# Kernel tuning notes

Measured on AMD Instinct MI355X. Metric: run time of the kernel, lower is better.

Reference implementation:

```python
import jax, jax.numpy as jnp
import numpy as np

N = 200000   # nodes
E = 6400000  # edges (avg degree 32)
F_IN = 128
N_CLASSES = 4
DIMS = [F_IN, 24, 12, 6, 4, 2]


def setup_inputs() -> dict:
    key = jax.random.key(0)
    ks = jax.random.split(key, 16)
    inp = {}
    inp['x'] = jax.random.normal(ks[0], (N, F_IN), dtype=jnp.float32)
    inp['edge_index'] = jax.random.randint(ks[1], (2, E), 0, N, dtype=jnp.int32)
    for i in range(5):
        fan_in = DIMS[i]
        inp[f'W{i+1}'] = jax.random.normal(ks[2 + i], (DIMS[i], DIMS[i + 1]), dtype=jnp.float32) / np.float32(np.sqrt(fan_in))
        inp[f'b{i+1}'] = jnp.zeros((DIMS[i + 1],), dtype=jnp.float32)
    inp['Wc'] = jax.random.normal(ks[8], (2, N_CLASSES), dtype=jnp.float32) / np.float32(np.sqrt(2.0))
    inp['bc'] = jnp.zeros((N_CLASSES,), dtype=jnp.float32)
    return inp


def _gcn_forward(x, row, col, norm, weights, biases, Wc, bc):
    h = x
    for W, b in zip(weights, biases):
        xl = h @ W                               # [N, d_out] linear transform first (d_out <= d_in)
        msg = norm[:, None] * xl[row]            # gather + normalize: [E+N, d_out]
        agg = jax.ops.segment_max(msg, col, num_segments=N)  # aggr='max'
        h = jnp.tanh(agg + b)
    out = h @ Wc + bc
    return out, h


def reference(x, edge_index, W1, b1, W2, b2, W3, b3, W4, b4, W5, b5, Wc, bc):
    loops = jnp.arange(N, dtype=edge_index.dtype)
    row = jnp.concatenate([edge_index[0], loops])  # source (with self loops)
    col = jnp.concatenate([edge_index[1], loops])  # target
    # symmetric GCN normalization on A + I
    deg = jax.ops.segment_sum(jnp.ones_like(col, dtype=jnp.float32), col, num_segments=N)
    dinv = jnp.where(deg > 0, jax.lax.rsqrt(deg), 0.0)
    norm = dinv[row] * dinv[col]                   # [E+N]
    weights = [W1, W2, W3, W4, W5]
    biases = [b1, b2, b3, b4, b5]
    return _gcn_forward(x, row, col, norm, weights, biases, Wc, bc)
```

## Files before the change

### kernel.cpp

```cpp
#include <hip/hip_runtime.h>
#include <cmath>

#define NN 200000
#define EE 6400000
#define CSH 8
#define BSZ 256
#define NBKT 782
#define GRID_A 512
#define BLK_A 256
#define RB_SHIFT 13
#define NRB 25

__device__ __forceinline__ unsigned int fenc(float f) {
    unsigned int u = __float_as_uint(f);
    return (u & 0x80000000u) ? ~u : (u | 0x80000000u);
}
__device__ __forceinline__ float fdec(unsigned int u) {
    unsigned int v = (u & 0x80000000u) ? (u & 0x7FFFFFFFu) : ~u;
    return __uint_as_float(v);
}


__global__ __launch_bounds__(BLK_A) void count_buckets_kernel(const int* __restrict__ col,
                                                              int* __restrict__ blkhist) {
    __shared__ int h[NBKT];
    for (int t = threadIdx.x; t < NBKT; t += BLK_A) h[t] = 0;
    __syncthreads();
    const int4* col4 = (const int4*)col;
    for (int i = blockIdx.x * BLK_A + threadIdx.x; i < EE / 4; i += GRID_A * BLK_A) {
        int4 c = col4[i];
        atomicAdd(&h[c.x >> CSH], 1);
        atomicAdd(&h[c.y >> CSH], 1);
        atomicAdd(&h[c.z >> CSH], 1);
        atomicAdd(&h[c.w >> CSH], 1);
    }
    __syncthreads();
    for (int t = threadIdx.x; t < NBKT; t += BLK_A) blkhist[blockIdx.x * NBKT + t] = h[t];
}

__global__ __launch_bounds__(GRID_A) void scan_cols_kernel(int* __restrict__ blkhist,
                                                           int* __restrict__ btot) {
    __shared__ int sc[GRID_A];
    int bkt = blockIdx.x, t = threadIdx.x;
    int v = blkhist[t * NBKT + bkt];
    sc[t] = v;
    __syncthreads();
    for (int off = 1; off < GRID_A; off <<= 1) {
        int add = (t >= off) ? sc[t - off] : 0;
        __syncthreads();
        sc[t] += add;
        __syncthreads();
    }
    blkhist[t * NBKT + bkt] = sc[t] - v;
    if (t == GRID_A - 1) btot[bkt] = sc[t];
}

__global__ __launch_bounds__(1024) void scan_btot_kernel(const int* __restrict__ btot,
                                                         int* __restrict__ bbase) {
    __shared__ int sc[1024];
    int t = threadIdx.x;
    int v = (t < NBKT) ? btot[t] : 0;
    sc[t] = v;
    __syncthreads();
    for (int off = 1; off < 1024; off <<= 1) {
        int add = (t >= off) ? sc[t - off] : 0;
        __syncthreads();
        sc[t] += add;
        __syncthreads();
    }
    if (t < NBKT) bbase[t] = sc[t] - v;
    if (t == NBKT - 1) bbase[NBKT] = sc[t];
}

__global__ __launch_bounds__(BLK_A) void place_pairs_kernel(const int* __restrict__ row,
                                                            const int* __restrict__ col,
                                                            const int* __restrict__ blkhist,
                                                            const int* __restrict__ bbase,
                                                            unsigned int* __restrict__ pairs) {
    __shared__ int cur[NBKT];
    for (int t = threadIdx.x; t < NBKT; t += BLK_A)
        cur[t] = bbase[t] + blkhist[blockIdx.x * NBKT + t];
    __syncthreads();
    const int4* col4 = (const int4*)col;
    const int4* row4 = (const int4*)row;
    for (int i = blockIdx.x * BLK_A + threadIdx.x; i < EE / 4; i += GRID_A * BLK_A) {
        int4 c = col4[i];
        int4 r = row4[i];
        int p0 = atomicAdd(&cur[c.x >> CSH], 1);
        pairs[p0] = (unsigned int)r.x | ((unsigned int)(c.x & (BSZ - 1)) << 18);
        int p1 = atomicAdd(&cur[c.y >> CSH], 1);
        pairs[p1] = (unsigned int)r.y | ((unsigned int)(c.y & (BSZ - 1)) << 18);
        int p2 = atomicAdd(&cur[c.z >> CSH], 1);
        pairs[p2] = (unsigned int)r.z | ((unsigned int)(c.z & (BSZ - 1)) << 18);
        int p3 = atomicAdd(&cur[c.w >> CSH], 1);
        pairs[p3] = (unsigned int)r.w | ((unsigned int)(c.w & (BSZ - 1)) << 18);
    }
}

__global__ __launch_bounds__(512) void bucket_build_band_kernel(const unsigned int* __restrict__ pairs,
                                                                const int* __restrict__ bbase,
                                                                float* __restrict__ dinv,
                                                                unsigned int* __restrict__ codes,
                                                                int* __restrict__ bandoffs) {
    __shared__ int bin[BSZ * NRB];
    __shared__ int sc[512];
    int b = blockIdx.x, tid = threadIdx.x;
    int base = bbase[b], end = bbase[b + 1];
    int node0 = b << CSH;
    int nloc = NN - node0; if (nloc > BSZ) nloc = BSZ;

    for (int t = tid; t < BSZ * NRB; t += 512) bin[t] = 0;
    __syncthreads();
    for (int i = base + tid; i < end; i += 512) {
        unsigned int p = pairs[i];
        int lc = p >> 18;
        int rw = (int)(p & 0x3FFFFu);
        atomicAdd(&bin[(rw >> RB_SHIFT) * BSZ + lc], 1);
    }
    __syncthreads();

    if (tid < nloc) {
        int d = 0;
#pragma unroll
        for (int bb = 0; bb < NRB; ++bb) d += bin[bb * BSZ + tid];
        dinv[node0 + tid] = rsqrtf((float)(d + 1));
    }
    __syncthreads();

    int tot = 0;
    if (tid < BSZ) {
#pragma unroll
        for (int i = 0; i < NRB; ++i) tot += bin[tid * NRB + i];
    }
    sc[tid] = tot;
    __syncthreads();
    for (int off = 1; off < 512; off <<= 1) {
        int add = (tid >= off) ? sc[tid - off] : 0;
        __syncthreads();
        sc[tid] += add;
        __syncthreads();
    }
    if (tid < BSZ) {
        int run = base + sc[tid] - tot;
#pragma unroll
        for (int i = 0; i < NRB; ++i) {
            int c = bin[tid * NRB + i];
            bin[tid * NRB + i] = run;
            run += c;
        }
    }
    __syncthreads();

    if (tid < NRB) bandoffs[b * (NRB + 1) + tid] = bin[tid * BSZ];
    if (tid == 0) bandoffs[b * (NRB + 1) + NRB] = end;
    __syncthreads();

    for (int i = base + tid; i < end; i += 512) {
        unsigned int p = pairs[i];
        int lc = p >> 18;
        int rw = (int)(p & 0x3FFFFu);
        int pos = atomicAdd(&bin[(rw >> RB_SHIFT) * BSZ + lc], 1);
        codes[pos] = p;
    }
}

__global__ void matmul128_y_kernel(const float* __restrict__ x, const float* __restrict__ W,
                                   const float* __restrict__ dinv, unsigned int* __restrict__ y, int n) {
    __shared__ float Ws[128 * 24];
    for (int t = threadIdx.x; t < 128 * 24; t += blockDim.x) Ws[t] = W[t];
    __syncthreads();
    int i = blockIdx.x * blockDim.x + threadIdx.x;
    if (i >= n) return;
    float acc[24];
#pragma unroll
    for (int j = 0; j < 24; ++j) acc[j] = 0.f;
    const float4* hr = (const float4*)(x + (size_t)i * 128);
#pragma unroll 8
    for (int k4 = 0; k4 < 32; ++k4) {
        float4 hv = hr[k4];
        const float* wk = &Ws[k4 * 4 * 24];
#pragma unroll
        for (int j = 0; j < 24; ++j) acc[j] += hv.x * wk[j];
#pragma unroll
        for (int j = 0; j < 24; ++j) acc[j] += hv.y * wk[24 + j];
#pragma unroll
        for (int j = 0; j < 24; ++j) acc[j] += hv.z * wk[48 + j];
#pragma unroll
        for (int j = 0; j < 24; ++j) acc[j] += hv.w * wk[72 + j];
    }
    float di = dinv[i];
    uint4* orow = (uint4*)(y + (size_t)i * 24);
#pragma unroll
    for (int q = 0; q < 6; ++q) {
        uint4 o;
        o.x = fenc(di * acc[q * 4 + 0]);
        o.y = fenc(di * acc[q * 4 + 1]);
        o.z = fenc(di * acc[q * 4 + 2]);
        o.w = fenc(di * acc[q * 4 + 3]);
        orow[q] = o;
    }
}

template<int DOUT, int DNEXT, bool FINAL, int PHASES>
__global__ __launch_bounds__(512) void gather_band_kernel(const unsigned int* __restrict__ codes,
                                                          const int* __restrict__ bandoffs,
                                                          const float* __restrict__ dinv,
                                                          const unsigned int* __restrict__ y,
                                                          const float* __restrict__ bias,
                                                          const float* __restrict__ Wn,
                                                          const float* __restrict__ bcls,
                                                          float* __restrict__ outp,
                                                          float* __restrict__ hout) {
    constexpr int ST = DOUT + 1;
    __shared__ unsigned int acc[BSZ * ST];
    __shared__ float dcs[BSZ];
    __shared__ float Ws[DOUT * DNEXT];
    __shared__ float bs[DOUT];
    const int b0 = blockIdx.x;
    const int node0 = b0 << CSH;
    const int nloc = (NN - node0 < BSZ) ? (NN - node0) : BSZ;
    const int tid = threadIdx.x;

    if (tid < DOUT * DNEXT) Ws[tid] = Wn[tid];
    if (tid < DOUT) bs[tid] = bias[tid];
    if (tid < nloc) dcs[tid] = dinv[node0 + tid];
    for (int idx = tid; idx < nloc * DOUT; idx += 512) {
        int lc = idx / DOUT;
        int f  = idx - lc * DOUT;
        acc[lc * ST + f] = y[(size_t)node0 * DOUT + idx];
    }
    __syncthreads();

    const int* bo = bandoffs + b0 * (NRB + 1);
#pragma unroll 1
    for (int ph = 0; ph < PHASES; ++ph) {
        const int s0 = (PHASES == 1) ? bo[0] : bo[ph];
        const int e  = (PHASES == 1) ? bo[NRB] : bo[ph + 1];
        for (int i = s0 + tid; i < e; i += 1024) {
            const int i2 = i + 512;
            const bool two = (i2 < e);
            unsigned int p0 = codes[i];
            size_t r0 = (size_t)(p0 & 0x3FFFFu);
            unsigned int* a0 = &acc[(p0 >> 18) * ST];
            unsigned int p1 = 0; unsigned int* a1 = nullptr;
            if constexpr (DOUT % 4 == 0) {
                constexpr int NQ = DOUT / 4;
                const uint4* y0 = (const uint4*)(y + r0 * DOUT);
                uint4 c0[NQ];
#pragma unroll
                for (int q = 0; q < NQ; ++q) c0[q] = y0[q];
                uint4 c1[NQ];
                if (two) {
                    p1 = codes[i2];
                    size_t r1 = (size_t)(p1 & 0x3FFFFu);
                    const uint4* y1 = (const uint4*)(y + r1 * DOUT);
#pragma unroll
                    for (int q = 0; q < NQ; ++q) c1[q] = y1[q];
                    a1 = &acc[(p1 >> 18) * ST];
                }
#pragma unroll
                for (int q = 0; q < NQ; ++q) {
                    if (c0[q].x > a0[q * 4 + 0]) atomicMax(&a0[q * 4 + 0], c0[q].x);
                    if (c0[q].y > a0[q * 4 + 1]) atomicMax(&a0[q * 4 + 1], c0[q].y);
                    if (c0[q].z > a0[q * 4 + 2]) atomicMax(&a0[q * 4 + 2], c0[q].z);
                    if (c0[q].w > a0[q * 4 + 3]) atomicMax(&a0[q * 4 + 3], c0[q].w);
                }
                if (two) {
#pragma unroll
                    for (int q = 0; q < NQ; ++q) {
                        if (c1[q].x > a1[q * 4 + 0]) atomicMax(&a1[q * 4 + 0], c1[q].x);
                        if (c1[q].y > a1[q * 4 + 1]) atomicMax(&a1[q * 4 + 1], c1[q].y);
                        if (c1[q].z > a1[q * 4 + 2]) atomicMax(&a1[q * 4 + 2], c1[q].z);
                        if (c1[q].w > a1[q * 4 + 3]) atomicMax(&a1[q * 4 + 3], c1[q].w);
                    }
                }
            } else {
                constexpr int NQ = DOUT / 2;
                const uint2* y0 = (const uint2*)(y + r0 * DOUT);
                uint2 c0[NQ];
#pragma unroll
                for (int q = 0; q < NQ; ++q) c0[q] = y0[q];
                uint2 c1[NQ];
                if (two) {
                    p1 = codes[i2];
                    size_t r1 = (size_t)(p1 & 0x3FFFFu);
                    const uint2* y1 = (const uint2*)(y + r1 * DOUT);
#pragma unroll
                    for (int q = 0; q < NQ; ++q) c1[q] = y1[q];
                    a1 = &acc[(p1 >> 18) * ST];
                }
#pragma unroll
                for (int q = 0; q < NQ; ++q) {
                    if (c0[q].x > a0[q * 2 + 0]) atomicMax(&a0[q * 2 + 0], c0[q].x);
                    if (c0[q].y > a0[q * 2 + 1]) atomicMax(&a0[q * 2 + 1], c0[q].y);
                }
                if (two) {
#pragma unroll
                    for (int q = 0; q < NQ; ++q) {
                        if (c1[q].x > a1[q * 2 + 0]) atomicMax(&a1[q * 2 + 0], c1[q].x);
                        if (c1[q].y > a1[q * 2 + 1]) atomicMax(&a1[q * 2 + 1], c1[q].y);
                    }
                }
            }
        }
        __syncthreads();
    }

    float* hsf = (float*)acc;
    for (int idx = tid; idx < nloc * DOUT; idx += 512) {
        int lc = idx / DOUT;
        int f  = idx - lc * DOUT;
        hsf[lc * ST + f] = tanhf(dcs[lc] * fdec(acc[lc * ST + f]) + bs[f]);
    }
    __syncthreads();

    if constexpr (!FINAL) {
        unsigned int* outu = (unsigned int*)outp;
        for (int idx = tid; idx < nloc * DNEXT; idx += 512) {
            int lc = idx / DNEXT;
            int j = idx - lc * DNEXT;
            float a = 0.f;
#pragma unroll
            for (int k = 0; k < DOUT; ++k) a += hsf[lc * ST + k] * Ws[k * DNEXT + j];
            outu[(size_t)node0 * DNEXT + idx] = fenc(dcs[lc] * a);
        }
    } else {
        for (int lc = tid; lc < nloc; lc += 512) {
            float h0 = hsf[lc * ST], h1 = hsf[lc * ST + 1];
            float2 ho; ho.x = h0; ho.y = h1;
            ((float2*)hout)[node0 + lc] = ho;
            float4 o;
            o.x = h0 * Ws[0] + h1 * Ws[DNEXT + 0] + bcls[0];
            o.y = h0 * Ws[1] + h1 * Ws[DNEXT + 1] + bcls[1];
            o.z = h0 * Ws[2] + h1 * Ws[DNEXT + 2] + bcls[2];
            o.w = h0 * Ws[3] + h1 * Ws[DNEXT + 3] + bcls[3];
            ((float4*)outp)[node0 + lc] = o;
        }
    }
}

extern "C" void kernel_launch(void* const* d_in, const int* in_sizes, int n_in,
                              void* d_out, int out_size, void* d_ws, size_t ws_size,
                              hipStream_t stream) {
    const float* x  = (const float*)d_in[0];
    const int*   ei = (const int*)d_in[1];
    const int* row = ei;
    const int* col = ei + EE;
    const float* W1 = (const float*)d_in[2];  const float* b1 = (const float*)d_in[3];
    const float* W2 = (const float*)d_in[4];  const float* b2 = (const float*)d_in[5];
    const float* W3 = (const float*)d_in[6];  const float* b3 = (const float*)d_in[7];
    const float* W4 = (const float*)d_in[8];  const float* b4 = (const float*)d_in[9];
    const float* W5 = (const float*)d_in[10]; const float* b5 = (const float*)d_in[11];
    const float* Wc = (const float*)d_in[12]; const float* bc = (const float*)d_in[13];
    float* out = (float*)d_out;

    char* ws = (char*)d_ws;
    float*        dinv       = (float*)(ws + 0);
    int*          bandoffs   = (int*)(ws + 800000);
    int*          bbase      = (int*)(ws + 881408);
    int*          btot       = (int*)(ws + 884608);
    int*          blkhist    = (int*)(ws + 887808);
    unsigned int* codes      = (unsigned int*)(ws + 2489344);
    unsigned int* pairs      = (unsigned int*)(ws + 28089344);
    unsigned int* bufB       = (unsigned int*)(ws + 28089344);
    unsigned int* bufA       = (unsigned int*)(ws + 53689344);

    const int BLK = 256;
    const int gN = (NN + BLK - 1) / BLK;

    count_buckets_kernel<<<GRID_A, BLK_A, 0, stream>>>(col, blkhist);
    scan_cols_kernel<<<NBKT, GRID_A, 0, stream>>>(blkhist, btot);
    scan_btot_kernel<<<1, 1024, 0, stream>>>(btot, bbase);
    place_pairs_kernel<<<GRID_A, BLK_A, 0, stream>>>(row, col, blkhist, bbase, pairs);
    bucket_build_band_kernel<<<NBKT, 512, 0, stream>>>(pairs, bbase, dinv, codes, bandoffs);

    matmul128_y_kernel<<<gN, BLK, 0, stream>>>(x, W1, dinv, bufB, NN);

    gather_band_kernel<24, 12, false, NRB><<<NBKT, 512, 0, stream>>>(
        codes, bandoffs, dinv, bufB, b1, W2, nullptr, (float*)bufA, nullptr);
    gather_band_kernel<12, 6, false, NRB><<<NBKT, 512, 0, stream>>>(
        codes, bandoffs, dinv, bufA, b2, W3, nullptr, (float*)bufB, nullptr);
    gather_band_kernel<6, 4, false, NRB><<<NBKT, 512, 0, stream>>>(
        codes, bandoffs, dinv, bufB, b3, W4, nullptr, (float*)bufA, nullptr);
    gather_band_kernel<4, 2, false, 1><<<NBKT, 512, 0, stream>>>(
        codes, bandoffs, dinv, bufA, b4, W5, nullptr, (float*)bufB, nullptr);
    gather_band_kernel<2, 4, true, 1><<<NBKT, 512, 0, stream>>>(
        codes, bandoffs, dinv, bufB, b5, Wc, bc, out, out + (size_t)NN * 4);
}
```

Baseline: 677.7 us.

## Store intermediate features as packed fp16 and max-reduce with CAS loop

Intermediate per-node features move from order-preserving encoded fp32 to packed fp16 pairs, with row strides padded (12->8->4->2->1 words) for vector loads. The LDS max aggregation now uses a CAS loop around v_pk_max_f16, handling two features per 32-bit word. The aim is to halve gather traffic and LDS atomic count. The cost is fp16 precision loss, CAS retries under contention, and the per-node epilogue now running on only one thread per node.

New measurement: 741.4 us. 1.09x slower.

```diff
diff --git a/kernel.cpp b/kernel.cpp
--- a/kernel.cpp
+++ b/kernel.cpp
@@ -1,4 +1,5 @@
 #include <hip/hip_runtime.h>
+#include <hip/hip_fp16.h>
 #include <cmath>
 
 #define NN 200000
@@ -11,13 +12,56 @@
 #define RB_SHIFT 13
 #define NRB 25
 
-__device__ __forceinline__ unsigned int fenc(float f) {
-    unsigned int u = __float_as_uint(f);
-    return (u & 0x80000000u) ? ~u : (u | 0x80000000u);
-}
-__device__ __forceinline__ float fdec(unsigned int u) {
-    unsigned int v = (u & 0x80000000u) ? (u & 0x7FFFFFFFu) : ~u;
-    return __uint_as_float(v);
+__device__ __forceinline__ unsigned int pkmax_f16(unsigned int a, unsigned int b) {
+    unsigned int r;
+    asm("v_pk_max_f16 %0, %1, %2" : "=v"(r) : "v"(a), "v"(b));
+    return r;
+}
+__device__ __forceinline__ void lds_max_f16(unsigned int* addr, unsigned int v) {
+    unsigned int cur = *addr;
+    unsigned int mx = pkmax_f16(cur, v);
+    while (mx != cur) {
+        unsigned int old = atomicCAS(addr, cur, mx);
+        if (old == cur) break;
+        cur = old;
+        mx = pkmax_f16(cur, v);
+    }
+}
+__device__ __forceinline__ float f16tof32(unsigned short s) {
+    union { unsigned short u; __half h; } cv; cv.u = s;
+    return __half2float(cv.h);
+}
+__device__ __forceinline__ float f16lo(unsigned int w) { return f16tof32((unsigned short)(w & 0xFFFFu)); }
+__device__ __forceinline__ float f16hi(unsigned int w) { return f16tof32((unsigned short)(w >> 16)); }
+__device__ __forceinline__ unsigned int pack16(float a, float b) {
+    union { __half2 h2; unsigned int u; } cv;
+    cv.h2 = __floats2half2_rn(a, b);
+    return cv.u;
+}
+
+template<int YW>
+__device__ __forceinline__ void loadrow(const unsigned int* __restrict__ y, size_t r,
+                                        unsigned int* cw) {
+    if constexpr (YW == 12) {
+        const uint4* p = (const uint4*)(y + r * 12);
+        uint4 a = p[0], b = p[1], c = p[2];
+        cw[0]=a.x; cw[1]=a.y; cw[2]=a.z; cw[3]=a.w;
+        cw[4]=b.x; cw[5]=b.y; cw[6]=b.z; cw[7]=b.w;
+        cw[8]=c.x; cw[9]=c.y; cw[10]=c.z; cw[11]=c.w;
+    } else if constexpr (YW == 8) {
+        const uint4* p = (const uint4*)(y + r * 8);
+        uint4 a = p[0], b = p[1];
+        cw[0]=a.x; cw[1]=a.y; cw[2]=a.z; cw[3]=a.w;
+        cw[4]=b.x; cw[5]=b.y; cw[6]=b.z; cw[7]=b.w;
+    } else if constexpr (YW == 4) {
+        uint4 a = *(const uint4*)(y + r * 4);
+        cw[0]=a.x; cw[1]=a.y; cw[2]=a.z; cw[3]=a.w;
+    } else if constexpr (YW == 2) {
+        uint2 a = *(const uint2*)(y + r * 2);
+        cw[0]=a.x; cw[1]=a.y;
+    } else {
+        cw[0] = y[r];
+    }
 }
 
 
@@ -189,19 +233,24 @@
         for (int j = 0; j < 24; ++j) acc[j] += hv.w * wk[72 + j];
     }
     float di = dinv[i];
-    uint4* orow = (uint4*)(y + (size_t)i * 24);
-#pragma unroll
-    for (int q = 0; q < 6; ++q) {
-        uint4 o;
-        o.x = fenc(di * acc[q * 4 + 0]);
-        o.y = fenc(di * acc[q * 4 + 1]);
-        o.z = fenc(di * acc[q * 4 + 2]);
-        o.w = fenc(di * acc[q * 4 + 3]);
-        orow[q] = o;
-    }
-}
-
-template<int DOUT, int DNEXT, bool FINAL, int PHASES>
+    uint4 o0, o1, o2;
+    o0.x = pack16(di * acc[0],  di * acc[1]);
+    o0.y = pack16(di * acc[2],  di * acc[3]);
+    o0.z = pack16(di * acc[4],  di * acc[5]);
+    o0.w = pack16(di * acc[6],  di * acc[7]);
+    o1.x = pack16(di * acc[8],  di * acc[9]);
+    o1.y = pack16(di * acc[10], di * acc[11]);
+    o1.z = pack16(di * acc[12], di * acc[13]);
+    o1.w = pack16(di * acc[14], di * acc[15]);
+    o2.x = pack16(di * acc[16], di * acc[17]);
+    o2.y = pack16(di * acc[18], di * acc[19]);
+    o2.z = pack16(di * acc[20], di * acc[21]);
+    o2.w = pack16(di * acc[22], di * acc[23]);
+    uint4* orow = (uint4*)(y + (size_t)i * 12);
+    orow[0] = o0; orow[1] = o1; orow[2] = o2;
+}
+
+template<int DOUT, int DNEXT, int YWI, int YWO, bool FINAL, int PHASES>
 __global__ __launch_bounds__(512) void gather_band_kernel(const unsigned int* __restrict__ codes,
                                                           const int* __restrict__ bandoffs,
                                                           const float* __restrict__ dinv,
@@ -209,9 +258,11 @@
                                                           const float* __restrict__ bias,
                                                           const float* __restrict__ Wn,
                                                           const float* __restrict__ bcls,
-                                                          float* __restrict__ outp,
+                                                          unsigned int* __restrict__ outp,
+                                                          float* __restrict__ fout,
                                                           float* __restrict__ hout) {
-    constexpr int ST = DOUT + 1;
+    constexpr int NW = DOUT / 2;
+    constexpr int ST = NW | 1;
     __shared__ unsigned int acc[BSZ * ST];
     __shared__ float dcs[BSZ];
     __shared__ float Ws[DOUT * DNEXT];
@@ -224,10 +275,10 @@
     if (tid < DOUT * DNEXT) Ws[tid] = Wn[tid];
     if (tid < DOUT) bs[tid] = bias[tid];
     if (tid < nloc) dcs[tid] = dinv[node0 + tid];
-    for (int idx = tid; idx < nloc * DOUT; idx += 512) {
-        int lc = idx / DOUT;
-        int f  = idx - lc * DOUT;
-        acc[lc * ST + f] = y[(size_t)node0 * DOUT + idx];
+    for (int idx = tid; idx < nloc * NW; idx += 512) {
+        int lc = idx / NW;
+        int w  = idx - lc * NW;
+        acc[lc * ST + w] = y[(size_t)(node0 + lc) * YWI + w];
     }
     __syncthreads();
 
@@ -242,99 +293,57 @@
             unsigned int p0 = codes[i];
             size_t r0 = (size_t)(p0 & 0x3FFFFu);
             unsigned int* a0 = &acc[(p0 >> 18) * ST];
-            unsigned int p1 = 0; unsigned int* a1 = nullptr;
-            if constexpr (DOUT % 4 == 0) {
-                constexpr int NQ = DOUT / 4;
-                const uint4* y0 = (const uint4*)(y + r0 * DOUT);
-                uint4 c0[NQ];
-#pragma unroll
-                for (int q = 0; q < NQ; ++q) c0[q] = y0[q];
-                uint4 c1[NQ];
-                if (two) {
-                    p1 = codes[i2];
-                    size_t r1 = (size_t)(p1 & 0x3FFFFu);
-                    const uint4* y1 = (const uint4*)(y + r1 * DOUT);
-#pragma unroll
-                    for (int q = 0; q < NQ; ++q) c1[q] = y1[q];
-                    a1 = &acc[(p1 >> 18) * ST];
-                }
-#pragma unroll
-                for (int q = 0; q < NQ; ++q) {
-                    if (c0[q].x > a0[q * 4 + 0]) atomicMax(&a0[q * 4 + 0], c0[q].x);
-                    if (c0[q].y > a0[q * 4 + 1]) atomicMax(&a0[q * 4 + 1], c0[q].y);
-                    if (c0[q].z > a0[q * 4 + 2]) atomicMax(&a0[q * 4 + 2], c0[q].z);
-                    if (c0[q].w > a0[q * 4 + 3]) atomicMax(&a0[q * 4 + 3], c0[q].w);
-                }
-                if (two) {
-#pragma unroll
-                    for (int q = 0; q < NQ; ++q) {
-                        if (c1[q].x > a1[q * 4 + 0]) atomicMax(&a1[q * 4 + 0], c1[q].x);
-                        if (c1[q].y > a1[q * 4 + 1]) atomicMax(&a1[q * 4 + 1], c1[q].y);
-                        if (c1[q].z > a1[q * 4 + 2]) atomicMax(&a1[q * 4 + 2], c1[q].z);
-                        if (c1[q].w > a1[q * 4 + 3]) atomicMax(&a1[q * 4 + 3], c1[q].w);
-                    }
-                }
-            } else {
-                constexpr int NQ = DOUT / 2;
-                const uint2* y0 = (const uint2*)(y + r0 * DOUT);
-                uint2 c0[NQ];
-#pragma unroll
-                for (int q = 0; q < NQ; ++q) c0[q] = y0[q];
-                uint2 c1[NQ];
-                if (two) {
-                    p1 = codes[i2];
-                    size_t r1 = (size_t)(p1 & 0x3FFFFu);
-                    const uint2* y1 = (const uint2*)(y + r1 * DOUT);
-#pragma unroll
-                    for (int q = 0; q < NQ; ++q) c1[q] = y1[q];
-                    a1 = &acc[(p1 >> 18) * ST];
-                }
-#pragma unroll
-                for (int q = 0; q < NQ; ++q) {
-                    if (c0[q].x > a0[q * 2 + 0]) atomicMax(&a0[q * 2 + 0], c0[q].x);
-                    if (c0[q].y > a0[q * 2 + 1]) atomicMax(&a0[q * 2 + 1], c0[q].y);
-                }
-                if (two) {
-#pragma unroll
-                    for (int q = 0; q < NQ; ++q) {
-                        if (c1[q].x > a1[q * 2 + 0]) atomicMax(&a1[q * 2 + 0], c1[q].x);
-                        if (c1[q].y > a1[q * 2 + 1]) atomicMax(&a1[q * 2 + 1], c1[q].y);
-                    }
-                }
+            unsigned int cw0[YWI], cw1[YWI];
+            loadrow<YWI>(y, r0, cw0);
+            unsigned int* a1 = nullptr;
+            if (two) {
+                unsigned int p1 = codes[i2];
+                loadrow<YWI>(y, (size_t)(p1 & 0x3FFFFu), cw1);
+                a1 = &acc[(p1 >> 18) * ST];
+            }
+#pragma unroll
+            for (int w = 0; w < NW; ++w) lds_max_f16(&a0[w], cw0[w]);
+            if (two) {
+#pragma unroll
+                for (int w = 0; w < NW; ++w) lds_max_f16(&a1[w], cw1[w]);
             }
         }
         __syncthreads();
     }
 
-    float* hsf = (float*)acc;
-    for (int idx = tid; idx < nloc * DOUT; idx += 512) {
-        int lc = idx / DOUT;
-        int f  = idx - lc * DOUT;
-        hsf[lc * ST + f] = tanhf(dcs[lc] * fdec(acc[lc * ST + f]) + bs[f]);
-    }
-    __syncthreads();
-
-    if constexpr (!FINAL) {
-        unsigned int* outu = (unsigned int*)outp;
-        for (int idx = tid; idx < nloc * DNEXT; idx += 512) {
-            int lc = idx / DNEXT;
-            int j = idx - lc * DNEXT;
-            float a = 0.f;
-#pragma unroll
-            for (int k = 0; k < DOUT; ++k) a += hsf[lc * ST + k] * Ws[k * DNEXT + j];
-            outu[(size_t)node0 * DNEXT + idx] = fenc(dcs[lc] * a);
+    if (tid < nloc) {
+        const int node = node0 + tid;
+        float dc = dcs[tid];
+        float h[DOUT];
+#pragma unroll
+        for (int w = 0; w < NW; ++w) {
+            unsigned int u = acc[tid * ST + w];
+            h[2 * w]     = f16lo(u);
+            h[2 * w + 1] = f16hi(u);
         }
-    } else {
-        for (int lc = tid; lc < nloc; lc += 512) {
-            float h0 = hsf[lc * ST], h1 = hsf[lc * ST + 1];
-            float2 ho; ho.x = h0; ho.y = h1;
-            ((float2*)hout)[node0 + lc] = ho;
+#pragma unroll
+        for (int f = 0; f < DOUT; ++f) h[f] = tanhf(dc * h[f] + bs[f]);
+        if constexpr (!FINAL) {
+            constexpr int NWO = DNEXT / 2;
+#pragma unroll
+            for (int jw = 0; jw < NWO; ++jw) {
+                float o0 = 0.f, o1 = 0.f;
+#pragma unroll
+                for (int k = 0; k < DOUT; ++k) {
+                    o0 += h[k] * Ws[k * DNEXT + 2 * jw];
+                    o1 += h[k] * Ws[k * DNEXT + 2 * jw + 1];
+                }
+                outp[(size_t)node * YWO + jw] = pack16(dc * o0, dc * o1);
+            }
+        } else {
+            float2 ho; ho.x = h[0]; ho.y = h[1];
+            ((float2*)hout)[node] = ho;
             float4 o;
-            o.x = h0 * Ws[0] + h1 * Ws[DNEXT + 0] + bcls[0];
-            o.y = h0 * Ws[1] + h1 * Ws[DNEXT + 1] + bcls[1];
-            o.z = h0 * Ws[2] + h1 * Ws[DNEXT + 2] + bcls[2];
-            o.w = h0 * Ws[3] + h1 * Ws[DNEXT + 3] + bcls[3];
-            ((float4*)outp)[node0 + lc] = o;
+            o.x = h[0] * Ws[0] + h[1] * Ws[DNEXT + 0] + bcls[0];
+            o.y = h[0] * Ws[1] + h[1] * Ws[DNEXT + 1] + bcls[1];
+            o.z = h[0] * Ws[2] + h[1] * Ws[DNEXT + 2] + bcls[2];
+            o.w = h[0] * Ws[3] + h[1] * Ws[DNEXT + 3] + bcls[3];
+            ((float4*)fout)[node] = o;
         }
     }
 }
@@ -376,14 +385,14 @@
 
     matmul128_y_kernel<<<gN, BLK, 0, stream>>>(x, W1, dinv, bufB, NN);
 
-    gather_band_kernel<24, 12, false, NRB><<<NBKT, 512, 0, stream>>>(
-        codes, bandoffs, dinv, bufB, b1, W2, nullptr, (float*)bufA, nullptr);
-    gather_band_kernel<12, 6, false, NRB><<<NBKT, 512, 0, stream>>>(
-        codes, bandoffs, dinv, bufA, b2, W3, nullptr, (float*)bufB, nullptr);
-    gather_band_kernel<6, 4, false, NRB><<<NBKT, 512, 0, stream>>>(
-        codes, bandoffs, dinv, bufB, b3, W4, nullptr, (float*)bufA, nullptr);
-    gather_band_kernel<4, 2, false, 1><<<NBKT, 512, 0, stream>>>(
-        codes, bandoffs, dinv, bufA, b4, W5, nullptr, (float*)bufB, nullptr);
-    gather_band_kernel<2, 4, true, 1><<<NBKT, 512, 0, stream>>>(
-        codes, bandoffs, dinv, bufB, b5, Wc, bc, out, out + (size_t)NN * 4);
-}
+    gather_band_kernel<24, 12, 12, 8, false, NRB><<<NBKT, 512, 0, stream>>>(
+        codes, bandoffs, dinv, bufB, b1, W2, nullptr, bufA, nullptr, nullptr);
+    gather_band_kernel<12, 6, 8, 4, false, NRB><<<NBKT, 512, 0, stream>>>(
+        codes, bandoffs, dinv, bufA, b2, W3, nullptr, bufB, nullptr, nullptr);
+    gather_band_kernel<6, 4, 4, 2, false, NRB><<<NBKT, 512, 0, stream>>>(
+        codes, bandoffs, dinv, bufB, b3, W4, nullptr, bufA, nullptr, nullptr);
+    gather_band_kernel<4, 2, 2, 1, false, 1><<<NBKT, 512, 0, stream>>>(
+        codes, bandoffs, dinv, bufA, b4, W5, nullptr, bufB, nullptr, nullptr);
+    gather_band_kernel<2, 4, 1, 1, true, 1><<<NBKT, 512, 0, stream>>>(
+        codes, bandoffs, dinv, bufB, b5, Wc, bc, nullptr, out, out + (size_t)NN * 4);
+}
```
